# Performance work log

Hardware: AMD Instinct MI355X
Metric: run time of the kernel (lower is better)

The kernel has to match this reference:

```python
import jax, jax.numpy as jnp
import numpy as np

N, E, G = 50000, 800000, 512
DIN, HID, DOUT, L, DE = 64, 64, 128, 3, 16
NEG_SLOPE = 0.2
BN_EPS = 1e-5


def setup_inputs() -> dict:
    key = jax.random.key(0)
    ks = jax.random.split(key, 20)
    s = 0.1  # weight scale for numerical stability
    return {
        "x": jax.random.normal(ks[0], (N, DIN), jnp.float32),
        "edge_index": jax.random.randint(ks[1], (2, E), 0, N, jnp.int32),
        "edge_attr": jax.random.normal(ks[2], (E, DE), jnp.float32),
        "batch": jnp.sort(jax.random.randint(ks[3], (N,), 0, G, jnp.int32)),
        "emb_W": jax.random.normal(ks[4], (HID, DIN), jnp.float32) * s,
        "emb_b": jax.random.normal(ks[5], (HID,), jnp.float32) * s,
        "Wl": jax.random.normal(ks[6], (L, HID, HID), jnp.float32) * s,
        "bl": jax.random.normal(ks[7], (L, HID), jnp.float32) * s,
        "Wr": jax.random.normal(ks[8], (L, HID, HID), jnp.float32) * s,
        "br": jax.random.normal(ks[9], (L, HID), jnp.float32) * s,
        "We": jax.random.normal(ks[10], (L, HID, DE), jnp.float32) * s,
        "att": jax.random.normal(ks[11], (L, HID), jnp.float32) * s,
        "conv_bias": jax.random.normal(ks[12], (L, HID), jnp.float32) * s,
        "bn_gamma": jax.random.uniform(ks[13], (L, HID), jnp.float32, 0.5, 1.5),
        "bn_beta": jax.random.normal(ks[14], (L, HID), jnp.float32) * s,
        "bn_mean": jnp.zeros((L, HID), jnp.float32),
        "bn_var": jnp.ones((L, HID), jnp.float32),
        "lin_W": jax.random.normal(ks[15], (DOUT, HID), jnp.float32) * s,
        "lin_b": jax.random.normal(ks[16], (DOUT,), jnp.float32) * s,
    }


def _gatv2(h, src, dst, edge_attr, Wl, bl, Wr, br, We, att, bias):
    # GATv2Conv, heads=1, concat=False, with edge features
    xl = h @ Wl.T + bl                      # [N,C] source transform (also message value)
    xr = h @ Wr.T + br                      # [N,C] target transform
    ea = edge_attr @ We.T                   # [E,C]
    m = xl[src] + xr[dst] + ea              # [E,C]
    m = jax.nn.leaky_relu(m, NEG_SLOPE)
    alpha = m @ att                         # [E] attention logits
    amax = jax.ops.segment_max(alpha, dst, num_segments=N)
    ea_exp = jnp.exp(alpha - amax[dst])
    denom = jax.ops.segment_sum(ea_exp, dst, num_segments=N)
    alpha = ea_exp / (denom[dst] + 1e-16)
    out = jax.ops.segment_sum(alpha[:, None] * xl[src], dst, num_segments=N)
    return out + bias


def reference(x, edge_index, edge_attr, batch, emb_W, emb_b, Wl, bl, Wr, br,
              We, att, conv_bias, bn_gamma, bn_beta, bn_mean, bn_var, lin_W, lin_b):
    src, dst = edge_index[0], edge_index[1]
    h = x @ emb_W.T + emb_b
    for i in range(L):
        hc = _gatv2(h, src, dst, edge_attr, Wl[i], bl[i], Wr[i], br[i],
                    We[i], att[i], conv_bias[i])
        # BatchNorm (eval mode, running stats)
        hc = (hc - bn_mean[i]) * jax.lax.rsqrt(bn_var[i] + BN_EPS) * bn_gamma[i] + bn_beta[i]
        hc = jax.nn.gelu(hc, approximate=False)  # torch F.gelu default is exact erf
        h = h + hc                                # residual; dropout p=0 / eval -> identity
    out = h @ lin_W.T + lin_b                     # [N,DOUT]
    counts = jax.ops.segment_sum(jnp.ones((N,), out.dtype), batch, num_segments=G)
    pooled = jax.ops.segment_sum(out, batch, num_segments=G)
    return pooled / jnp.maximum(counts, 1.0)[:, None]
```

## Files before the change

kernel.cpp:

```cpp
#include <hip/hip_runtime.h>
#include <math.h>

#define NEG_SLOPE 0.2f
#define BN_EPS 1e-5f

template <int N> struct IC { static constexpr int v = N; };
template <bool B> struct BC { static constexpr bool v = B; };

typedef _Float16 half2v __attribute__((ext_vector_type(2)));

__device__ __forceinline__ half2v u2h(unsigned u) {
  union { unsigned u; half2v h; } c;
  c.u = u;
  return c.h;
}
__device__ __forceinline__ unsigned pkh(float lo, float hi) {
  union { half2v h; unsigned u; } c;
  c.h[0] = (_Float16)lo;
  c.h[1] = (_Float16)hi;
  return c.u;
}

#if defined(__has_builtin)
#if __has_builtin(__builtin_amdgcn_fdot2)
#define FDOT2(a, b, c) __builtin_amdgcn_fdot2((a), (b), (c), false)
#endif
#endif
#ifndef FDOT2
__device__ __forceinline__ float fdot2_sw(half2v a, half2v b, float c) {
  return c + (float)a[0] * (float)b[0] + (float)a[1] * (float)b[1];
}
#define FDOT2(a, b, c) fdot2_sw((a), (b), (c))
#endif

#define FMA4(acc, v, wq) \
  acc += (v).x * (wq).x + (v).y * (wq).y + (v).z * (wq).z + (v).w * (wq).w

#define DOT_ROW(buf, r, bias, OUT)                                     \
  {                                                                    \
    __builtin_amdgcn_sched_barrier(0);                                 \
    float a0 = 0.f, a1 = 0.f, a2 = 0.f, a3 = 0.f;                      \
    _Pragma("unroll") for (int q = 0; q < 4; q++) {                    \
      float4 v0 = *(const float4*)((buf) + (r) * 64 + q * 16 + 0);     \
      float4 v1 = *(const float4*)((buf) + (r) * 64 + q * 16 + 4);     \
      float4 v2 = *(const float4*)((buf) + (r) * 64 + q * 16 + 8);     \
      float4 v3 = *(const float4*)((buf) + (r) * 64 + q * 16 + 12);    \
      FMA4(a0, v0, W[q * 4 + 0]);                                      \
      FMA4(a1, v1, W[q * 4 + 1]);                                      \
      FMA4(a2, v2, W[q * 4 + 2]);                                      \
      FMA4(a3, v3, W[q * 4 + 3]);                                      \
    }                                                                  \
    OUT = (bias) + ((a0 + a1) + (a2 + a3));                            \
  }

__device__ __forceinline__ float wave_sum64(float v) {
  int x;
  x = __builtin_amdgcn_update_dpp(0, __float_as_int(v), 0x121, 0xF, 0xF, true);
  v += __int_as_float(x);
  x = __builtin_amdgcn_update_dpp(0, __float_as_int(v), 0x122, 0xF, 0xF, true);
  v += __int_as_float(x);
  x = __builtin_amdgcn_update_dpp(0, __float_as_int(v), 0x124, 0xF, 0xF, true);
  v += __int_as_float(x);
  x = __builtin_amdgcn_update_dpp(0, __float_as_int(v), 0x128, 0xF, 0xF, true);
  v += __int_as_float(x);
  v += __shfl_xor(v, 16, 64);
  v += __shfl_xor(v, 32, 64);
  return v;
}

__global__ __launch_bounds__(256) void hist_kernel(
    const int* __restrict__ dst, const int* __restrict__ batch,
    int* __restrict__ deg, float* __restrict__ counts, int E_, int N_) {
  int i = blockIdx.x * 256 + threadIdx.x;
  if (i < E_) atomicAdd(&deg[dst[i]], 1);
  if (i < N_) atomicAdd(&counts[batch[i]], 1.0f);
}

__global__ __launch_bounds__(256) void scanA_kernel(
    const int* __restrict__ deg, int* __restrict__ row_ptr,
    int* __restrict__ segTot, int N_, int nseg) {
  __shared__ int sb[256];
  int t = threadIdx.x;
  for (int s = blockIdx.x; s < nseg; s += gridDim.x) {
    int i = s * 256 + t;
    int v = (i < N_) ? deg[i] : 0;
    sb[t] = v;
    __syncthreads();
    for (int off = 1; off < 256; off <<= 1) {
      int a = (t >= off) ? sb[t - off] : 0;
      __syncthreads();
      sb[t] += a;
      __syncthreads();
    }
    int incl = sb[t];
    if (i < N_) row_ptr[i] = incl - v;
    if (t == 255) segTot[s] = incl;
    __syncthreads();
  }
}

__global__ __launch_bounds__(256) void scanB_kernel(int* __restrict__ segTot,
                                                    int nseg) {
  __shared__ int sb[256];
  __shared__ int baseSh;
  int t = threadIdx.x;
  if (t == 0) baseSh = 0;
  __syncthreads();
  for (int c0 = 0; c0 < nseg; c0 += 256) {
    int s = c0 + t;
    int v = (s < nseg) ? segTot[s] : 0;
    sb[t] = v;
    __syncthreads();
    for (int off = 1; off < 256; off <<= 1) {
      int a = (t >= off) ? sb[t - off] : 0;
      __syncthreads();
      sb[t] += a;
      __syncthreads();
    }
    int incl = sb[t];
    int base = baseSh;
    if (s < nseg) segTot[s] = base + incl - v;
    __syncthreads();
    if (t == 255) baseSh = base + incl;
    __syncthreads();
  }
}

__global__ __launch_bounds__(256) void scanC_kernel(
    int* __restrict__ row_ptr, const int* __restrict__ segTot,
    int* __restrict__ cursor, int N_, int E_) {
  int tid = blockIdx.x * 256 + threadIdx.x;
  int nt = gridDim.x * 256;
  for (int i = tid; i < N_; i += nt) {
    int rp = row_ptr[i] + segTot[i >> 8];
    row_ptr[i] = rp;
    cursor[i] = rp;
  }
  if (tid == 0) row_ptr[N_] = E_;
}

__global__ __launch_bounds__(256) void scatter_kernel(
    const int* __restrict__ src, const int* __restrict__ dst,
    const float4* __restrict__ edge_attr4, int* __restrict__ cursor,
    int* __restrict__ csr_src, int* __restrict__ csr_eid,
    unsigned* __restrict__ attr_u, int E_) {
  int e = blockIdx.x * 256 + threadIdx.x;
  if (e >= E_) return;
  int pos = atomicAdd(&cursor[dst[e]], 1);
  csr_src[pos] = src[e];
  if (attr_u) {
    float4 a0 = edge_attr4[e * 4 + 0];
    float4 a1 = edge_attr4[e * 4 + 1];
    float4 a2 = edge_attr4[e * 4 + 2];
    float4 a3 = edge_attr4[e * 4 + 3];
    uint4 u0, u1;
    u0.x = pkh(a0.x, a0.y);
    u0.y = pkh(a0.z, a0.w);
    u0.z = pkh(a1.x, a1.y);
    u0.w = pkh(a1.z, a1.w);
    u1.x = pkh(a2.x, a2.y);
    u1.y = pkh(a2.z, a2.w);
    u1.z = pkh(a3.x, a3.y);
    u1.w = pkh(a3.z, a3.w);
    uint4* d4 = (uint4*)(attr_u + (size_t)pos * 8);
    d4[0] = u0;
    d4[1] = u1;
  } else {
    csr_eid[pos] = e;
  }
}

__global__ __launch_bounds__(256, 3) void emb_lin0_kernel(
    const float* __restrict__ x, const float* __restrict__ emb_W,
    const float* __restrict__ emb_b, const float* __restrict__ Wl0,
    const float* __restrict__ bl0, const float* __restrict__ Wr0,
    const float* __restrict__ br0, float* __restrict__ h,
    _Float16* __restrict__ xl, _Float16* __restrict__ xr, int rows) {
  __shared__ float sx[4096];
  __shared__ float sh[4096];
  int lane = threadIdx.x & 63;
  int w = threadIdx.x >> 6;
  int n0 = blockIdx.x * 64;

  {
    int gmax = rows * 64 - 4;
#pragma unroll
    for (int i = 0; i < 4; i++) {
      int off = w * 1024 + i * 256 + lane * 4;
      int g = min(n0 * 64 + off, gmax);
      *(float4*)(sx + off) = *(const float4*)(x + g);
    }
  }

  float4 W[16];
  float b;

#pragma unroll
  for (int q = 0; q < 16; q++) W[q] = ((const float4*)(emb_W + lane * 64))[q];
  b = emb_b[lane];
#pragma unroll 1
  for (int t = 0; t < 16; t++) {
    int r = w * 16 + t;
    float a;
    DOT_ROW(sx, r, b, a);
    sh[r * 64 + lane] = a;
    int n = n0 + r;
    if (n < rows) h[(size_t)n * 64 + lane] = a;
  }

#pragma unroll
  for (int q = 0; q < 16; q++) W[q] = ((const float4*)(Wl0 + lane * 64))[q];
  b = bl0[lane];
#pragma unroll 1
  for (int t = 0; t < 16; t++) {
    int r = w * 16 + t;
    float a;
    DOT_ROW(sh, r, b, a);
    int n = n0 + r;
    if (n < rows) xl[(size_t)n * 64 + lane] = (_Float16)a;
  }

#pragma unroll
  for (int q = 0; q < 16; q++) W[q] = ((const float4*)(Wr0 + lane * 64))[q];
  b = br0[lane];
#pragma unroll 1
  for (int t = 0; t < 16; t++) {
    int r = w * 16 + t;
    float a;
    DOT_ROW(sh, r, b, a);
    int n = n0 + r;
    if (n < rows) xr[(size_t)n * 64 + lane] = (_Float16)a;
  }
}

__global__ __launch_bounds__(256, 3) void linx2_kernel(
    const float* __restrict__ in, const float* __restrict__ Wl,
    const float* __restrict__ bl, const float* __restrict__ Wr,
    const float* __restrict__ br, _Float16* __restrict__ xl,
    _Float16* __restrict__ xr, int rows) {
  __shared__ float sx[4096];
  int lane = threadIdx.x & 63;
  int w = threadIdx.x >> 6;
  int n0 = blockIdx.x * 64;

  {
    int gmax = rows * 64 - 4;
#pragma unroll
    for (int i = 0; i < 4; i++) {
      int off = w * 1024 + i * 256 + lane * 4;
      int g = min(n0 * 64 + off, gmax);
      *(float4*)(sx + off) = *(const float4*)(in + g);
    }
  }

  float4 W[16];
  float b;

#pragma unroll
  for (int q = 0; q < 16; q++) W[q] = ((const float4*)(Wl + lane * 64))[q];
  b = bl[lane];
#pragma unroll 1
  for (int t = 0; t < 16; t++) {
    int r = w * 16 + t;
    float a;
    DOT_ROW(sx, r, b, a);
    int n = n0 + r;
    if (n < rows) xl[(size_t)n * 64 + lane] = (_Float16)a;
  }

#pragma unroll
  for (int q = 0; q < 16; q++) W[q] = ((const float4*)(Wr + lane * 64))[q];
  b = br[lane];
#pragma unroll 1
  for (int t = 0; t < 16; t++) {
    int r = w * 16 + t;
    float a;
    DOT_ROW(sx, r, b, a);
    int n = n0 + r;
    if (n < rows) xr[(size_t)n * 64 + lane] = (_Float16)a;
  }
}

template <bool CONTIG>
__global__ __launch_bounds__(256) void gat_fused_kernel(
    const int* __restrict__ csr_src, const int* __restrict__ csr_eid,
    const int* __restrict__ row_ptr, const unsigned* __restrict__ attr_u,
    const float* __restrict__ edge_attr, const _Float16* __restrict__ xl,
    const _Float16* __restrict__ xr, const float* __restrict__ We,
    const float* __restrict__ att, const float* __restrict__ conv_bias,
    const float* __restrict__ gamma, const float* __restrict__ beta,
    const float* __restrict__ mean, const float* __restrict__ var,
    float* __restrict__ h, int N_) {
  int d = (blockIdx.x * 256 + threadIdx.x) >> 6;
  if (d >= N_) return;
  int j = threadIdx.x & 63;
  half2v Wek2[8];
  float Wekf[16];
  if constexpr (CONTIG) {
#pragma unroll
    for (int q = 0; q < 8; q++) {
      Wek2[q][0] = (_Float16)We[j * 16 + 2 * q];
      Wek2[q][1] = (_Float16)We[j * 16 + 2 * q + 1];
    }
  } else {
#pragma unroll
    for (int k = 0; k < 16; k++) Wekf[k] = We[j * 16 + k];
  }
  float att_j = att[j];
  float sc = rsqrtf(var[j] + BN_EPS) * gamma[j];
  float sh = (conv_bias[j] - mean[j]) * sc + beta[j];

  int beg = __builtin_amdgcn_readfirstlane(row_ptr[d]);
  int end = __builtin_amdgcn_readfirstlane(row_ptr[d + 1]);
  float xrj = (float)xr[(size_t)d * 64 + j];
  float m = -INFINITY, l = 0.f, acc = 0.f;

  auto chunk = [&](int base, auto C_, auto PAD_) {
    constexpr int C = decltype(C_)::v;
    constexpr bool PAD = decltype(PAD_)::v;
    int si[C];
#pragma unroll
    for (int t = 0; t < C; t++) {
      int idx = PAD ? min(base + t, end - 1) : (base + t);
      si[t] = csr_src[idx];
    }
    float xlv[C];
#pragma unroll
    for (int t = 0; t < C; t++)
      xlv[t] = (float)xl[(size_t)si[t] * 64 + j];
    float v[C];
#pragma unroll
    for (int t = 0; t < C; t++) {
      int idx = PAD ? min(base + t, end - 1) : (base + t);
      float ea;
      if constexpr (CONTIG) {
        const uint4* ap = (const uint4*)(attr_u + (size_t)idx * 8);
        uint4 ua = ap[0], ub = ap[1];
        ea = 0.f;
        ea = FDOT2(u2h(ua.x), Wek2[0], ea);
        ea = FDOT2(u2h(ua.y), Wek2[1], ea);
        ea = FDOT2(u2h(ua.z), Wek2[2], ea);
        ea = FDOT2(u2h(ua.w), Wek2[3], ea);
        ea = FDOT2(u2h(ub.x), Wek2[4], ea);
        ea = FDOT2(u2h(ub.y), Wek2[5], ea);
        ea = FDOT2(u2h(ub.z), Wek2[6], ea);
        ea = FDOT2(u2h(ub.w), Wek2[7], ea);
      } else {
        const float4* ap =
            (const float4*)(edge_attr + (size_t)csr_eid[idx] * 16);
        float4 a0 = ap[0], a1 = ap[1], a2 = ap[2], a3 = ap[3];
        ea = a0.x * Wekf[0]  + a0.y * Wekf[1]  + a0.z * Wekf[2]  + a0.w * Wekf[3]
           + a1.x * Wekf[4]  + a1.y * Wekf[5]  + a1.z * Wekf[6]  + a1.w * Wekf[7]
           + a2.x * Wekf[8]  + a2.y * Wekf[9]  + a2.z * Wekf[10] + a2.w * Wekf[11]
           + a3.x * Wekf[12] + a3.y * Wekf[13] + a3.z * Wekf[14] + a3.w * Wekf[15];
      }
      float z = xlv[t] + xrj + ea;
      z = fmaxf(z, NEG_SLOPE * z);
      float p = wave_sum64(z * att_j);
      v[t] = (!PAD || (base + t < end)) ? p : -INFINITY;
    }
    float mc = v[0];
#pragma unroll
    for (int t = 1; t < C; t++) mc = fmaxf(mc, v[t]);
    float newm = fmaxf(m, mc);
    float s = __expf(m - newm);
    l *= s;
    acc *= s;
#pragma unroll
    for (int t = 0; t < C; t++) {
      float w = __expf(v[t] - newm);
      l += w;
      acc += w * xlv[t];
    }
    m = newm;
  };

  int base = beg;
  for (; base + 16 <= end; base += 16) chunk(base, IC<16>{}, BC<false>{});
  if (base + 8 <= end) {
    chunk(base, IC<8>{}, BC<false>{});
    base += 8;
  }
  if (base < end) chunk(base, IC<8>{}, BC<true>{});

  float val = acc / (l + 1e-16f) * sc + sh;
  float g = 0.5f * val * (1.f + erff(val * 0.70710678118654752f));
  h[(size_t)d * 64 + j] += g;
}

__global__ __launch_bounds__(256, 2) void lin_pool_kernel(
    const float* __restrict__ h, const float* __restrict__ lin_W,
    const float* __restrict__ lin_b, const int* __restrict__ batch,
    const float* __restrict__ counts, float* __restrict__ pooled, int rows) {
  __shared__ float shh[4096];
  int lane = threadIdx.x & 63;
  int w = threadIdx.x >> 6;
  int n0 = blockIdx.x * 64;

  {
    int gmax = rows * 64 - 4;
#pragma unroll
    for (int i = 0; i < 4; i++) {
      int off = w * 1024 + i * 256 + lane * 4;
      int g = min(n0 * 64 + off, gmax);
      *(float4*)(shh + off) = *(const float4*)(h + g);
    }
  }

  float4 W0[16], W1[16];
#pragma unroll
  for (int q = 0; q < 16; q++) W0[q] = ((const float4*)(lin_W + lane * 64))[q];
#pragma unroll
  for (int q = 0; q < 16; q++)
    W1[q] = ((const float4*)(lin_W + (lane + 64) * 64))[q];
  float b0 = lin_b[lane], b1 = lin_b[lane + 64];

  int curg = -1;
  float acc0 = 0.f, acc1 = 0.f;
  int lim = min(16, rows - n0 - w * 16);
#pragma unroll 1
  for (int t = 0; t < lim; t++) {
    int r = w * 16 + t;
    __builtin_amdgcn_sched_barrier(0);
    float d0 = b0, d1 = b1;
#pragma unroll
    for (int q = 0; q < 16; q++) {
      float4 v = *(const float4*)(shh + r * 64 + q * 4);
      FMA4(d0, v, W0[q]);
      FMA4(d1, v, W1[q]);
    }
    int g = batch[n0 + r];
    if (g != curg) {
      if (curg >= 0) {
        float inv = 1.f / fmaxf(counts[curg], 1.f);
        atomicAdd(&pooled[curg * 128 + lane], acc0 * inv);
        atomicAdd(&pooled[curg * 128 + 64 + lane], acc1 * inv);
      }
      curg = g;
      acc0 = 0.f;
      acc1 = 0.f;
    }
    acc0 += d0;
    acc1 += d1;
  }
  if (curg >= 0) {
    float inv = 1.f / fmaxf(counts[curg], 1.f);
    atomicAdd(&pooled[curg * 128 + lane], acc0 * inv);
    atomicAdd(&pooled[curg * 128 + 64 + lane], acc1 * inv);
  }
}

extern "C" void kernel_launch(void* const* d_in, const int* in_sizes, int n_in,
                              void* d_out, int out_size, void* d_ws, size_t ws_size,
                              hipStream_t stream) {
  const float* x         = (const float*)d_in[0];
  const int*   edge_index= (const int*)  d_in[1];
  const float* edge_attr = (const float*)d_in[2];
  const int*   batch     = (const int*)  d_in[3];
  const float* emb_W     = (const float*)d_in[4];
  const float* emb_b     = (const float*)d_in[5];
  const float* Wl        = (const float*)d_in[6];
  const float* bl        = (const float*)d_in[7];
  const float* Wr        = (const float*)d_in[8];
  const float* br        = (const float*)d_in[9];
  const float* We        = (const float*)d_in[10];
  const float* att       = (const float*)d_in[11];
  const float* conv_bias = (const float*)d_in[12];
  const float* bn_gamma  = (const float*)d_in[13];
  const float* bn_beta   = (const float*)d_in[14];
  const float* bn_mean   = (const float*)d_in[15];
  const float* bn_var    = (const float*)d_in[16];
  const float* lin_W     = (const float*)d_in[17];
  const float* lin_b     = (const float*)d_in[18];

  const int N_ = in_sizes[0] / 64;
  const int E_ = in_sizes[1] / 2;
  const int G_ = out_size / 128;
  const int* src = edge_index;
  const int* dst = edge_index + E_;

  const int Npad = (N_ + 3) & ~3;
  const int Epad = (E_ + 19) & ~3;
  const int nseg = (N_ + 255) / 256;

  float* ws      = (float*)d_ws;
  float* h       = ws;
  _Float16* xl   = (_Float16*)(h + (size_t)N_ * 64);
  _Float16* xr   = xl + (size_t)N_ * 64;
  int*   csr_src = (int*)(xr + (size_t)N_ * 64);
  int*   csr_eid = csr_src + Epad;
  int*   row_ptr = csr_eid + Epad;
  int*   cursor  = row_ptr + (Npad + 4);
  int*   deg     = cursor + Npad;
  float* counts  = (float*)(deg + Npad);
  int*   segTot  = (int*)(counts + G_);
  uintptr_t abp  = (uintptr_t)(segTot + nseg + 8);
  abp = (abp + 15) & ~(uintptr_t)15;
  unsigned* attr_u = (unsigned*)abp;

  size_t base_bytes = (abp - (uintptr_t)d_ws);
  bool contig = ws_size >= base_bytes + (size_t)E_ * 32 + 64;

  const int hgrid = (max(E_, N_) + 255) / 256;
  const int ngrid = (N_ + 255) / 256;

  hipMemsetAsync(deg, 0, ((size_t)Npad + G_) * 4, stream);
  hist_kernel<<<hgrid, 256, 0, stream>>>(dst, batch, deg, counts, E_, N_);
  scanA_kernel<<<min(nseg, 1024), 256, 0, stream>>>(deg, row_ptr, segTot, N_,
                                                    nseg);
  scanB_kernel<<<1, 256, 0, stream>>>(segTot, nseg);
  scanC_kernel<<<ngrid, 256, 0, stream>>>(row_ptr, segTot, cursor, N_, E_);
  scatter_kernel<<<(E_ + 255) / 256, 256, 0, stream>>>(
      src, dst, (const float4*)edge_attr, cursor, csr_src, csr_eid,
      contig ? attr_u : (unsigned*)nullptr, E_);

  const int tgrid = (N_ + 63) / 64;
  emb_lin0_kernel<<<tgrid, 256, 0, stream>>>(x, emb_W, emb_b, Wl, bl, Wr, br,
                                             h, xl, xr, N_);

  const int gatBlocks = (N_ + 3) / 4;
  for (int l = 0; l < 3; l++) {
    if (l > 0) {
      linx2_kernel<<<tgrid, 256, 0, stream>>>(
          h, Wl + (size_t)l * 4096, bl + l * 64, Wr + (size_t)l * 4096,
          br + l * 64, xl, xr, N_);
    }
    if (contig) {
      gat_fused_kernel<true><<<gatBlocks, 256, 0, stream>>>(
          csr_src, csr_eid, row_ptr, attr_u, edge_attr, xl, xr,
          We + (size_t)l * 1024, att + l * 64, conv_bias + l * 64,
          bn_gamma + l * 64, bn_beta + l * 64, bn_mean + l * 64,
          bn_var + l * 64, h, N_);
    } else {
      gat_fused_kernel<false><<<gatBlocks, 256, 0, stream>>>(
          csr_src, csr_eid, row_ptr, attr_u, edge_attr, xl, xr,
          We + (size_t)l * 1024, att + l * 64, conv_bias + l * 64,
          bn_gamma + l * 64, bn_beta + l * 64, bn_mean + l * 64,
          bn_var + l * 64, h, N_);
    }
  }

  hipMemsetAsync(d_out, 0, (size_t)G_ * 128 * 4, stream);
  lin_pool_kernel<<<(N_ + 63) / 64, 256, 0, stream>>>(
      h, lin_W, lin_b, batch, counts, (float*)d_out, N_);
}
```

Before: 621.8 us.

## Fuse Wl/Wr dot products, split attr permutation kernel, use exp2 softmax

Three changes in one. The linear kernels now compute the Wl and Wr projections together in one pass over each shared-memory row, halving LDS reads at the cost of twice the weight registers (launch bounds relaxed from 3 to 2 blocks per SM). The edge-attribute fp16 packing moves out of the atomic scatter into a separate kernel that writes sequentially in CSR order, adding one launch and a gather read of the attributes. The softmax folds log2(e) into the attention weight and uses exp2f instead of __expf.

```diff
diff --git a/kernel.cpp b/kernel.cpp
--- a/kernel.cpp
+++ b/kernel.cpp
@@ -51,6 +51,29 @@
       FMA4(a3, v3, W[q * 4 + 3]);                                      \
     }                                                                  \
     OUT = (bias) + ((a0 + a1) + (a2 + a3));                            \
+  }
+
+#define DOT_ROW2(buf, r, biasL, biasR, OUTL, OUTR)                     \
+  {                                                                    \
+    __builtin_amdgcn_sched_barrier(0);                                 \
+    float l0 = 0.f, l1 = 0.f, l2 = 0.f, l3 = 0.f;                      \
+    float r0 = 0.f, r1 = 0.f, r2 = 0.f, r3 = 0.f;                      \
+    _Pragma("unroll") for (int q = 0; q < 4; q++) {                    \
+      float4 v0 = *(const float4*)((buf) + (r) * 64 + q * 16 + 0);     \
+      float4 v1 = *(const float4*)((buf) + (r) * 64 + q * 16 + 4);     \
+      float4 v2 = *(const float4*)((buf) + (r) * 64 + q * 16 + 8);     \
+      float4 v3 = *(const float4*)((buf) + (r) * 64 + q * 16 + 12);    \
+      FMA4(l0, v0, WL[q * 4 + 0]);                                     \
+      FMA4(r0, v0, WR[q * 4 + 0]);                                     \
+      FMA4(l1, v1, WL[q * 4 + 1]);                                     \
+      FMA4(r1, v1, WR[q * 4 + 1]);                                     \
+      FMA4(l2, v2, WL[q * 4 + 2]);                                     \
+      FMA4(r2, v2, WR[q * 4 + 2]);                                     \
+      FMA4(l3, v3, WL[q * 4 + 3]);                                     \
+      FMA4(r3, v3, WR[q * 4 + 3]);                                     \
+    }                                                                  \
+    OUTL = (biasL) + ((l0 + l1) + (l2 + l3));                          \
+    OUTR = (biasR) + ((r0 + r1) + (r2 + r3));                          \
   }
 
 __device__ __forceinline__ float wave_sum64(float v) {
@@ -141,36 +164,40 @@
 
 __global__ __launch_bounds__(256) void scatter_kernel(
     const int* __restrict__ src, const int* __restrict__ dst,
-    const float4* __restrict__ edge_attr4, int* __restrict__ cursor,
-    int* __restrict__ csr_src, int* __restrict__ csr_eid,
-    unsigned* __restrict__ attr_u, int E_) {
+    int* __restrict__ cursor, int* __restrict__ csr_src,
+    int* __restrict__ csr_eid, int E_) {
   int e = blockIdx.x * 256 + threadIdx.x;
   if (e >= E_) return;
   int pos = atomicAdd(&cursor[dst[e]], 1);
   csr_src[pos] = src[e];
-  if (attr_u) {
-    float4 a0 = edge_attr4[e * 4 + 0];
-    float4 a1 = edge_attr4[e * 4 + 1];
-    float4 a2 = edge_attr4[e * 4 + 2];
-    float4 a3 = edge_attr4[e * 4 + 3];
-    uint4 u0, u1;
-    u0.x = pkh(a0.x, a0.y);
-    u0.y = pkh(a0.z, a0.w);
-    u0.z = pkh(a1.x, a1.y);
-    u0.w = pkh(a1.z, a1.w);
-    u1.x = pkh(a2.x, a2.y);
-    u1.y = pkh(a2.z, a2.w);
-    u1.z = pkh(a3.x, a3.y);
-    u1.w = pkh(a3.z, a3.w);
-    uint4* d4 = (uint4*)(attr_u + (size_t)pos * 8);
-    d4[0] = u0;
-    d4[1] = u1;
-  } else {
-    csr_eid[pos] = e;
-  }
-}
-
-__global__ __launch_bounds__(256, 3) void emb_lin0_kernel(
+  csr_eid[pos] = e;
+}
+
+__global__ __launch_bounds__(256) void permute_attr_kernel(
+    const float4* __restrict__ edge_attr4, const int* __restrict__ csr_eid,
+    unsigned* __restrict__ attr_u, int E_) {
+  int p = blockIdx.x * 256 + threadIdx.x;
+  if (p >= E_) return;
+  int e = csr_eid[p];
+  float4 a0 = edge_attr4[(size_t)e * 4 + 0];
+  float4 a1 = edge_attr4[(size_t)e * 4 + 1];
+  float4 a2 = edge_attr4[(size_t)e * 4 + 2];
+  float4 a3 = edge_attr4[(size_t)e * 4 + 3];
+  uint4 u0, u1;
+  u0.x = pkh(a0.x, a0.y);
+  u0.y = pkh(a0.z, a0.w);
+  u0.z = pkh(a1.x, a1.y);
+  u0.w = pkh(a1.z, a1.w);
+  u1.x = pkh(a2.x, a2.y);
+  u1.y = pkh(a2.z, a2.w);
+  u1.z = pkh(a3.x, a3.y);
+  u1.w = pkh(a3.z, a3.w);
+  uint4* d4 = (uint4*)(attr_u + (size_t)p * 8);
+  d4[0] = u0;
+  d4[1] = u1;
+}
+
+__global__ __launch_bounds__(256, 2) void emb_lin0_kernel(
     const float* __restrict__ x, const float* __restrict__ emb_W,
     const float* __restrict__ emb_b, const float* __restrict__ Wl0,
     const float* __restrict__ bl0, const float* __restrict__ Wr0,
@@ -192,48 +219,44 @@
     }
   }
 
-  float4 W[16];
-  float b;
-
-#pragma unroll
-  for (int q = 0; q < 16; q++) W[q] = ((const float4*)(emb_W + lane * 64))[q];
-  b = emb_b[lane];
+  {
+    float4 W[16];
+#pragma unroll
+    for (int q = 0; q < 16; q++) W[q] = ((const float4*)(emb_W + lane * 64))[q];
+    float b = emb_b[lane];
 #pragma unroll 1
-  for (int t = 0; t < 16; t++) {
-    int r = w * 16 + t;
-    float a;
-    DOT_ROW(sx, r, b, a);
-    sh[r * 64 + lane] = a;
-    int n = n0 + r;
-    if (n < rows) h[(size_t)n * 64 + lane] = a;
-  }
-
-#pragma unroll
-  for (int q = 0; q < 16; q++) W[q] = ((const float4*)(Wl0 + lane * 64))[q];
-  b = bl0[lane];
+    for (int t = 0; t < 16; t++) {
+      int r = w * 16 + t;
+      float a;
+      DOT_ROW(sx, r, b, a);
+      sh[r * 64 + lane] = a;
+      int n = n0 + r;
+      if (n < rows) h[(size_t)n * 64 + lane] = a;
+    }
+  }
+
+  {
+    float4 WL[16], WR[16];
+#pragma unroll
+    for (int q = 0; q < 16; q++) WL[q] = ((const float4*)(Wl0 + lane * 64))[q];
+#pragma unroll
+    for (int q = 0; q < 16; q++) WR[q] = ((const float4*)(Wr0 + lane * 64))[q];
+    float bL = bl0[lane], bR = br0[lane];
 #pragma unroll 1
-  for (int t = 0; t < 16; t++) {
-    int r = w * 16 + t;
-    float a;
-    DOT_ROW(sh, r, b, a);
-    int n = n0 + r;
-    if (n < rows) xl[(size_t)n * 64 + lane] = (_Float16)a;
-  }
-
-#pragma unroll
-  for (int q = 0; q < 16; q++) W[q] = ((const float4*)(Wr0 + lane * 64))[q];
-  b = br0[lane];
-#pragma unroll 1
-  for (int t = 0; t < 16; t++) {
-    int r = w * 16 + t;
-    float a;
-    DOT_ROW(sh, r, b, a);
-    int n = n0 + r;
-    if (n < rows) xr[(size_t)n * 64 + lane] = (_Float16)a;
-  }
-}
-
-__global__ __launch_bounds__(256, 3) void linx2_kernel(
+    for (int t = 0; t < 16; t++) {
+      int r = w * 16 + t;
+      float al, ar;
+      DOT_ROW2(sh, r, bL, bR, al, ar);
+      int n = n0 + r;
+      if (n < rows) {
+        xl[(size_t)n * 64 + lane] = (_Float16)al;
+        xr[(size_t)n * 64 + lane] = (_Float16)ar;
+      }
+    }
+  }
+}
+
+__global__ __launch_bounds__(256, 2) void linx2_kernel(
     const float* __restrict__ in, const float* __restrict__ Wl,
     const float* __restrict__ bl, const float* __restrict__ Wr,
     const float* __restrict__ br, _Float16* __restrict__ xl,
@@ -253,31 +276,22 @@
     }
   }
 
-  float4 W[16];
-  float b;
-
-#pragma unroll
-  for (int q = 0; q < 16; q++) W[q] = ((const float4*)(Wl + lane * 64))[q];
-  b = bl[lane];
+  float4 WL[16], WR[16];
+#pragma unroll
+  for (int q = 0; q < 16; q++) WL[q] = ((const float4*)(Wl + lane * 64))[q];
+#pragma unroll
+  for (int q = 0; q < 16; q++) WR[q] = ((const float4*)(Wr + lane * 64))[q];
+  float bL = bl[lane], bR = br[lane];
 #pragma unroll 1
   for (int t = 0; t < 16; t++) {
     int r = w * 16 + t;
-    float a;
-    DOT_ROW(sx, r, b, a);
+    float al, ar;
+    DOT_ROW2(sx, r, bL, bR, al, ar);
     int n = n0 + r;
-    if (n < rows) xl[(size_t)n * 64 + lane] = (_Float16)a;
-  }
-
-#pragma unroll
-  for (int q = 0; q < 16; q++) W[q] = ((const float4*)(Wr + lane * 64))[q];
-  b = br[lane];
-#pragma unroll 1
-  for (int t = 0; t < 16; t++) {
-    int r = w * 16 + t;
-    float a;
-    DOT_ROW(sx, r, b, a);
-    int n = n0 + r;
-    if (n < rows) xr[(size_t)n * 64 + lane] = (_Float16)a;
+    if (n < rows) {
+      xl[(size_t)n * 64 + lane] = (_Float16)al;
+      xr[(size_t)n * 64 + lane] = (_Float16)ar;
+    }
   }
 }
 
@@ -306,7 +320,7 @@
 #pragma unroll
     for (int k = 0; k < 16; k++) Wekf[k] = We[j * 16 + k];
   }
-  float att_j = att[j];
+  float att_j = att[j] * 1.44269504088896f;
   float sc = rsqrtf(var[j] + BN_EPS) * gamma[j];
   float sh = (conv_bias[j] - mean[j]) * sc + beta[j];
 
@@ -363,12 +377,12 @@
 #pragma unroll
     for (int t = 1; t < C; t++) mc = fmaxf(mc, v[t]);
     float newm = fmaxf(m, mc);
-    float s = __expf(m - newm);
+    float s = exp2f(m - newm);
     l *= s;
     acc *= s;
 #pragma unroll
     for (int t = 0; t < C; t++) {
-      float w = __expf(v[t] - newm);
+      float w = exp2f(v[t] - newm);
       l += w;
       acc += w * xlv[t];
     }
@@ -503,6 +517,7 @@
 
   const int hgrid = (max(E_, N_) + 255) / 256;
   const int ngrid = (N_ + 255) / 256;
+  const int egrid = (E_ + 255) / 256;
 
   hipMemsetAsync(deg, 0, ((size_t)Npad + G_) * 4, stream);
   hist_kernel<<<hgrid, 256, 0, stream>>>(dst, batch, deg, counts, E_, N_);
@@ -510,9 +525,12 @@
                                                     nseg);
   scanB_kernel<<<1, 256, 0, stream>>>(segTot, nseg);
   scanC_kernel<<<ngrid, 256, 0, stream>>>(row_ptr, segTot, cursor, N_, E_);
-  scatter_kernel<<<(E_ + 255) / 256, 256, 0, stream>>>(
-      src, dst, (const float4*)edge_attr, cursor, csr_src, csr_eid,
-      contig ? attr_u : (unsigned*)nullptr, E_);
+  scatter_kernel<<<egrid, 256, 0, stream>>>(src, dst, cursor, csr_src,
+                                            csr_eid, E_);
+  if (contig) {
+    permute_attr_kernel<<<egrid, 256, 0, stream>>>(
+        (const float4*)edge_attr, csr_eid, attr_u, E_);
+  }
 
   const int tgrid = (N_ + 63) / 64;
   emb_lin0_kernel<<<tgrid, 256, 0, stream>>>(x, emb_W, emb_b, Wl, bl, Wr, br,
```

After: 663.1 us. 1.07x slower.
